# Optimization experiments

Measured on AMD Instinct MI355X. Metric: run time of the kernel, lower is better.

Reference implementation:

```python
import jax, jax.numpy as jnp
import numpy as np

# ---- static skeleton structure (SMPL 24-joint, 23-edge kinematic tree) ----
SMPL_EDGES = [[0,1],[0,2],[0,3],[1,4],[2,5],[3,6],[4,7],[5,8],[6,9],[7,10],
              [8,11],[9,12],[9,13],[9,14],[12,15],[13,16],[14,17],[16,18],
              [17,19],[18,20],[19,21],[20,22],[21,23]]
KERNEL, STRIDE, PAD, DIST = 15, 2, 7, 1

def _edge_dist(edges):
    E = len(edges)
    m = np.full((E, E), 1e6)
    np.fill_diagonal(m, 0.0)
    for i, a in enumerate(edges):
        for j, b in enumerate(edges):
            if i != j and set(a) & set(b):
                m[i, j] = 1.0
    for k in range(E):  # Floyd-Warshall on the edge adjacency graph
        m = np.minimum(m, m[:, k:k+1] + m[k:k+1, :])
    return m

def _find_neighbor(edges, d, n_global):
    m = _edge_dist(edges); E = len(edges)
    nb = [list(np.nonzero(m[i] <= d)[0]) for i in range(E)]
    gp = list(nb[0])  # edges near root edge (keeps deep-motion-editing's known quirk)
    g_ids = [E + k for k in range(n_global)]
    for i in gp:
        nb[i].extend(g_ids)
    for _ in range(n_global):
        nb.append(gp + g_ids)
    return nb

def _find_seqs(edges):
    deg = {}
    for a, b in edges:
        deg[a] = deg.get(a, 0) + 1
        deg[b] = deg.get(b, 0) + 1
    seqs = []
    def rec(j, seq):
        if deg.get(j, 0) > 2 and j != 0:
            seqs.append(seq); seq = []
        if deg.get(j, 0) == 1:
            seqs.append(seq); return
        for idx, (a, b) in enumerate(edges):
            if a == j:
                rec(b, seq + [idx])
    rec(0, [])
    return seqs

def _pooling(edges, last_pool, global_ids):
    pools, new_edges = [], []
    for seq in _find_seqs(edges):
        if last_pool:
            pools.append(seq); continue
        if len(seq) % 2 == 1:
            pools.append([seq[0]]); new_edges.append(edges[seq[0]]); seq = seq[1:]
        for i in range(0, len(seq), 2):
            pools.append([seq[i], seq[i+1]])
            new_edges.append([edges[seq[i]][0], edges[seq[i+1]][1]])
    pools.append(list(global_ids))
    return pools, new_edges

def _conv_mask(nb, in_per, out_per):
    N = len(nb)
    mask = np.zeros((N*out_per, N*in_per, 1), np.float32)
    for i, ns in enumerate(nb):
        for j in ns:
            mask[i*out_per:(i+1)*out_per, j*in_per:(j+1)*in_per, 0] = 1.0
    return mask

def _pool_matrix(pools, n_nodes, cpe):
    W = np.zeros((len(pools)*cpe, n_nodes*cpe), np.float32)
    c = np.arange(cpe)
    for i, grp in enumerate(pools):
        for j in grp:
            W[i*cpe + c, j*cpe + c] = 1.0 / len(grp)
    return W

E0 = len(SMPL_EDGES)
N0 = E0 + 2  # 23 edges + global position node + root-velocity node (the '+4' channels)
MASK0 = jnp.asarray(_conv_mask(_find_neighbor(SMPL_EDGES, DIST, 2), 4, 8))  # (200,100,1)
_pools0, EDGES1 = _pooling(SMPL_EDGES, False, [E0, E0 + 1])
P0 = jnp.asarray(_pool_matrix(_pools0, N0, 8))  # (112,200)
N1 = len(EDGES1) + 1
MASK1 = jnp.asarray(_conv_mask(_find_neighbor(EDGES1, DIST, 1), 8, 16))  # (224,112,1)
_pools1, _ = _pooling(EDGES1, True, [N1 - 1])
P1 = jnp.asarray(_pool_matrix(_pools1, N1, 16))  # (112,224)

IN0, OUT0 = 4 * N0, 8 * N0    # 100, 200
IN1, OUT1 = 8 * N1, 16 * N1   # 112, 224
B, T_IN = 64, 2047            # 2048 frames after zero-frame append


def _skel_conv(x, w, b, mask):
    # masked Conv1d (skeleton-sparse weights), stride 2, zero padding 7, k=15
    y = jax.lax.conv_general_dilated(x, w * mask, window_strides=(STRIDE,),
                                     padding=[(PAD, PAD)],
                                     dimension_numbers=('NCH', 'OIH', 'NCH'))
    return y + b[None, :, None]


def _forward(x, w0, b0, w1, b1):
    # x: (B, T, C); append one zero frame on time dim, then to (B, C, T+1)
    out = jnp.concatenate([x, jnp.zeros_like(x[:, :1, :])], axis=1)
    out = out.transpose(0, 2, 1)
    out = jax.nn.relu(jnp.einsum('pc,bct->bpt', P0, _skel_conv(out, w0, b0, MASK0)))
    out = jax.nn.relu(jnp.einsum('pc,bct->bpt', P1, _skel_conv(out, w1, b1, MASK1)))
    return out  # (B, 112, (T+1)//4)


def setup_inputs() -> dict:
    key = jax.random.key(0)
    k = jax.random.split(key, 5)
    s = 0.05
    return {
        'x':  jax.random.normal(k[0], (B, T_IN, IN0), jnp.float32),
        'w0': jax.random.normal(k[1], (OUT0, IN0, KERNEL), jnp.float32) * s,
        'b0': jax.random.normal(k[2], (OUT0,), jnp.float32) * s,
        'w1': jax.random.normal(k[3], (OUT1, IN1, KERNEL), jnp.float32) * s,
        'b1': jax.random.normal(k[4], (OUT1,), jnp.float32) * s,
    }


def reference(x, w0, b0, w1, b1):
    return _forward(x, w0, b0, w1, b1)
```

## Files before the change

kernel.cpp:

```cpp
#include <hip/hip_runtime.h>


#define OFF_A2  107520u
#define OFF_BF0 322560u
#define OFF_BF1 323008u

typedef unsigned int uint32;
typedef __attribute__((ext_vector_type(8))) short bs8;
typedef __attribute__((ext_vector_type(4))) float f32x4;
union U8 { uint4 u; bs8 s; };

__constant__ int c_pool0_len[14] = {2,2,2,2,1,2,2,1,2,2,1,2,2,2};
__constant__ int c_pool0_mem[14][2] = {{0,3},{6,9},{1,4},{7,10},{2,2},{5,8},{11,14},{12,12},
                                       {15,17},{19,21},{13,13},{16,18},{20,22},{23,24}};
__constant__ unsigned c_nbm0[25] = {
 0x180000Fu,0x1800017u,0x1800027u,0x1800049u,0x92u,0x124u,0x248u,0x490u,
 0x3920u,0x240u,0x480u,0x7900u,0xB900u,0x13900u,0x4800u,0x29000u,
 0x52000u,0xA8000u,0x150000u,0x2A0000u,0x540000u,0x280000u,0x500000u,
 0x180000Fu,0x180000Fu
};
__constant__ int c_pool1_len[7] = {2,2,2,1,3,3,1};
__constant__ int c_pool1_mem[7][3] = {{0,1,1},{2,3,3},{4,5,5},{6,6,6},{7,8,9},{10,11,12},{13,13,13}};
__constant__ unsigned c_nbm1[14] = {
 0x2017u,0x2003u,0x201Du,0xCu,0x2035u,0x4F0u,0x4E0u,0x5E0u,
 0x380u,0x300u,0xCE0u,0x1C00u,0x1800u,0x2017u
};
__constant__ int c_g1p[7][2] = {{0,13},{1,3},{2,4},{5,6},{7,10},{8,11},{9,12}};
__constant__ int c_U1[7][8] = {
 {0,1,2,3,6,23,24,25},
 {3,4,6,7,9,10,25,25},
 {0,1,2,4,5,7,23,24},
 {2,5,8,11,12,13,14,25},
 {8,11,12,13,15,16,25,25},
 {12,13,15,16,17,18,19,20},
 {17,18,19,20,21,22,25,25}};
__constant__ int c_U2[7][8] = {
 {0,1,2,4,13,14,14,14},
 {0,2,3,4,13,14,14,14},
 {0,2,4,5,6,7,10,13},
 {5,6,7,10,14,14,14,14},
 {5,6,7,8,9,10,14,14},
 {5,6,7,10,11,12,14,14},
 {0,1,2,4,13,14,14,14}};
__constant__ unsigned c_pk1a[7] = {0xC0301000u,0xC8483018u,0xB8281000u,0x70604010u,
                                   0xC8786040u,0x98887860u,0xC8A89888u};
__constant__ unsigned c_pk1b[7] = {0xC8B81808u,0xC8503820u,0xC0382008u,0xC8685828u,
                                   0xC8806858u,0xA0908068u,0xC8B0A090u};
__constant__ unsigned c_pk2[7][2] = {
 {0x40201000u,0xE0E0E0D0u},{0x40302000u,0xE0E0E0D0u},{0x50402000u,0xD0A07060u},
 {0xA0706050u,0xE0E0E0E0u},{0x80706050u,0xE0E0A090u},{0xA0706050u,0xE0E0C0B0u},
 {0x40201000u,0xE0E0E0D0u}};

__device__ __forceinline__ uint32 f2bf(float v) {
  uint32 u = __float_as_uint(v);
  return (u + 0x7fffu + ((u >> 16) & 1u)) >> 16;
}

__global__ void prep_fused_weights(const float* __restrict__ w0, const float* __restrict__ b0,
                                   const float* __restrict__ w1, const float* __restrict__ b1,
                                   char* __restrict__ wsb) {
  int t = blockIdx.x * blockDim.x + threadIdx.x;
  if (t < 6720) {
    int lane = t & 63;
    int r = t >> 6;
    int k = r % 15, g = r / 15;
    int m = lane & 15, h = lane >> 4;
    int pool = (m < 8) ? c_g1p[g][0] : c_g1p[g][1];
    int c = m & 7;
    int L = c_pool0_len[pool];
    float inv = 1.f / (float)L;
    uint32 us[8];
#pragma unroll
    for (int j = 0; j < 8; ++j) {
      int node = c_U1[g][2 * h + (j >> 2)];
      int ci = j & 3;
      float v = 0.f;
      if (node < 25) {
        for (int jj = 0; jj < L; ++jj) {
          int mem = c_pool0_mem[pool][jj];
          if ((c_nbm0[mem] >> node) & 1u)
            v += w0[(mem * 8 + c) * 1500 + (node * 4 + ci) * 15 + k];
        }
        v *= inv;
      }
      us[j] = f2bf(v);
    }
    uint4 o = make_uint4(us[0] | (us[1] << 16), us[2] | (us[3] << 16),
                         us[4] | (us[5] << 16), us[6] | (us[7] << 16));
    reinterpret_cast<uint4*>(wsb)[t] = o;
  } else if (t < 6720 + 13440) {
    int t2 = t - 6720;
    int lane = t2 & 63;
    int r = t2 >> 6;
    int k = r % 15;
    int r2 = r / 15;
    int ks = r2 & 1, p = r2 >> 1;
    int c = lane & 15, h = lane >> 4;
    int node = c_U2[p][ks * 4 + h];
    int L = c_pool1_len[p];
    float inv = 1.f / (float)L;
    uint32 us[8];
#pragma unroll
    for (int j = 0; j < 8; ++j) {
      float v = 0.f;
      if (node < 14) {
        for (int jj = 0; jj < L; ++jj) {
          int mem = c_pool1_mem[p][jj];
          if ((c_nbm1[mem] >> node) & 1u)
            v += w1[(mem * 16 + c) * 1680 + (node * 8 + j) * 15 + k];
        }
        v *= inv;
      }
      us[j] = f2bf(v);
    }
    uint4 o = make_uint4(us[0] | (us[1] << 16), us[2] | (us[3] << 16),
                         us[4] | (us[5] << 16), us[6] | (us[7] << 16));
    reinterpret_cast<uint4*>(wsb + OFF_A2)[t2] = o;
  } else if (t < 6720 + 13440 + 112) {
    int p = t - (6720 + 13440);
    int i = p >> 3, c = p & 7;
    int L = c_pool0_len[i];
    float v = 0.f;
    for (int jj = 0; jj < L; ++jj) v += b0[c_pool0_mem[i][jj] * 8 + c];
    reinterpret_cast<float*>(wsb + OFF_BF0)[p] = v / (float)L;
  } else if (t < 6720 + 13440 + 224) {
    int p = t - (6720 + 13440 + 112);
    int i = p >> 4, c = p & 15;
    int L = c_pool1_len[i];
    float v = 0.f;
    for (int jj = 0; jj < L; ++jj) v += b1[c_pool1_mem[i][jj] * 16 + c];
    reinterpret_cast<float*>(wsb + OFF_BF1)[p] = v / (float)L;
  }
}

__global__ __launch_bounds__(448, 4) void conv_fused(const float* __restrict__ x,
                                                     const char* __restrict__ wsb,
                                                     float* __restrict__ out) {
  __shared__ __align__(16) unsigned char xs[173 * 256];
  __shared__ __align__(16) unsigned char ys[80 * 256];
  const int tid = threadIdx.x;
  const int lane = tid & 63;
  const int g = tid >> 6;
  const int m16 = lane & 15, h = lane >> 4;
  const int b = blockIdx.y;
  const int t0 = blockIdx.x << 5;
  const int f0y = 2 * t0 - 7;
  const int g0x = 4 * t0 - 21;

  const float* __restrict__ xb = x + (size_t)b * (2047 * 100);
  float4 rg[10];
#pragma unroll
  for (int i = 0; i < 10; ++i) {
    rg[i] = make_float4(0.f, 0.f, 0.f, 0.f);
    int e = tid + i * 448;
    if (e < 4325) {
      int f = e / 25, q = e - f * 25;
      int gt = g0x + f;
      if ((unsigned)gt < 2047u)
        rg[i] = *reinterpret_cast<const float4*>(xb + gt * 100 + 4 * q);
    }
  }
  for (int e = tid; e < 173; e += 448)
    *reinterpret_cast<uint2*>(xs + e * 256 + (200u ^ (((e >> 1) & 15) << 3))) =
        make_uint2(0u, 0u);
#pragma unroll
  for (int i = 0; i < 10; ++i) {
    int e = tid + i * 448;
    if (e < 4325) {
      int f = e / 25, q = e - f * 25;
      uint2 w = make_uint2(f2bf(rg[i].x) | (f2bf(rg[i].y) << 16),
                           f2bf(rg[i].z) | (f2bf(rg[i].w) << 16));
      *reinterpret_cast<uint2*>(xs + f * 256 + ((q * 8) ^ (((f >> 1) & 15) << 3))) = w;
    }
  }
  const uint4* __restrict__ A1p = reinterpret_cast<const uint4*>(wsb) + g * 960 + lane;
  U8 aw[15];
#pragma unroll
  for (int k = 0; k < 15; ++k) aw[k].u = A1p[k * 64];
  const int pa = c_g1p[g][0], pb = c_g1p[g][1];
  const int chbase = (h < 2) ? (pa * 8 + 4 * h) : (pb * 8 + 4 * (h - 2));
  const float4 bv0 = *reinterpret_cast<const float4*>(wsb + OFF_BF0 + chbase * 4);
  __syncthreads();

  const uint32 offA = (c_pk1a[g] >> (8 * h)) & 255u;
  const uint32 offB = (c_pk1b[g] >> (8 * h)) & 255u;
  f32x4 acc1[5];
#pragma unroll
  for (int nt = 0; nt < 5; ++nt) acc1[nt] = (f32x4)0.f;
#pragma unroll
  for (int k = 0; k < 15; ++k) {
    const uint32 sw = (uint32)(((m16 + (k >> 1)) & 15) << 3);
    const uint32 a0 = offA ^ sw, a1o = offB ^ sw;
    const unsigned char* base = xs + (2 * m16 + k) * 256;
#pragma unroll
    for (int nt = 0; nt < 5; ++nt) {
      uint2 lo = *reinterpret_cast<const uint2*>(base + nt * 8192 + a0);
      uint2 hi = *reinterpret_cast<const uint2*>(base + nt * 8192 + a1o);
      U8 bfr; bfr.u = make_uint4(lo.x, lo.y, hi.x, hi.y);
      acc1[nt] = __builtin_amdgcn_mfma_f32_16x16x32_bf16(aw[k].s, bfr.s, acc1[nt], 0, 0, 0);
    }
  }

  const uint4* __restrict__ A2p =
      reinterpret_cast<const uint4*>(wsb + OFF_A2) + g * 1920 + lane;
#pragma unroll
  for (int k = 0; k < 15; ++k) aw[k].u = A2p[k * 64];
  const float4 bv1 = *reinterpret_cast<const float4*>(wsb + OFF_BF1 + (g * 16 + 4 * h) * 4);

#pragma unroll
  for (int nt = 0; nt < 5; ++nt) {
    int row = nt * 16 + m16;
    int fy = f0y + row;
    float o0 = fmaxf(acc1[nt][0] + bv0.x, 0.f);
    float o1 = fmaxf(acc1[nt][1] + bv0.y, 0.f);
    float o2 = fmaxf(acc1[nt][2] + bv0.z, 0.f);
    float o3 = fmaxf(acc1[nt][3] + bv0.w, 0.f);
    uint2 wpk = make_uint2(f2bf(o0) | (f2bf(o1) << 16), f2bf(o2) | (f2bf(o3) << 16));
    if ((unsigned)fy >= 1024u) wpk = make_uint2(0u, 0u);
    *reinterpret_cast<uint2*>(ys + row * 256 +
        (((uint32)(chbase * 2)) ^ (((row >> 1) & 7) << 4))) = wpk;
  }
  for (int e = tid; e < 80; e += 448)
    *reinterpret_cast<uint4*>(ys + e * 256 + (224u ^ (((e >> 1) & 7) << 4))) =
        make_uint4(0u, 0u, 0u, 0u);
  __syncthreads();

  f32x4 acc2[2];
  acc2[0] = (f32x4)0.f; acc2[1] = (f32x4)0.f;
  {
    const uint32 noff = (c_pk2[g][0] >> (8 * h)) & 255u;
#pragma unroll
    for (int k = 0; k < 15; ++k) {
      const uint32 sw = (uint32)(((m16 + (k >> 1)) & 7) << 4);
      const unsigned char* base = ys + 2 * m16 * 256 + (noff ^ sw);
      U8 b0f, b1f;
      b0f.u = *reinterpret_cast<const uint4*>(base + k * 256);
      b1f.u = *reinterpret_cast<const uint4*>(base + (k + 32) * 256);
      acc2[0] = __builtin_amdgcn_mfma_f32_16x16x32_bf16(aw[k].s, b0f.s, acc2[0], 0, 0, 0);
      acc2[1] = __builtin_amdgcn_mfma_f32_16x16x32_bf16(aw[k].s, b1f.s, acc2[1], 0, 0, 0);
    }
  }
#pragma unroll
  for (int k = 0; k < 15; ++k) aw[k].u = A2p[(15 + k) * 64];
  {
    const uint32 noff = (c_pk2[g][1] >> (8 * h)) & 255u;
#pragma unroll
    for (int k = 0; k < 15; ++k) {
      const uint32 sw = (uint32)(((m16 + (k >> 1)) & 7) << 4);
      const unsigned char* base = ys + 2 * m16 * 256 + (noff ^ sw);
      U8 b0f, b1f;
      b0f.u = *reinterpret_cast<const uint4*>(base + k * 256);
      b1f.u = *reinterpret_cast<const uint4*>(base + (k + 32) * 256);
      acc2[0] = __builtin_amdgcn_mfma_f32_16x16x32_bf16(aw[k].s, b0f.s, acc2[0], 0, 0, 0);
      acc2[1] = __builtin_amdgcn_mfma_f32_16x16x32_bf16(aw[k].s, b1f.s, acc2[1], 0, 0, 0);
    }
  }

#pragma unroll
  for (int nt = 0; nt < 2; ++nt) {
    size_t obase = ((size_t)b * 112 + g * 16 + 4 * h) * 512 + t0 + nt * 16 + m16;
    out[obase]        = fmaxf(acc2[nt][0] + bv1.x, 0.f);
    out[obase + 512]  = fmaxf(acc2[nt][1] + bv1.y, 0.f);
    out[obase + 1024] = fmaxf(acc2[nt][2] + bv1.z, 0.f);
    out[obase + 1536] = fmaxf(acc2[nt][3] + bv1.w, 0.f);
  }
}

extern "C" void kernel_launch(void* const* d_in, const int* in_sizes, int n_in,
                              void* d_out, int out_size, void* d_ws, size_t ws_size,
                              hipStream_t stream) {
  const float* x  = (const float*)d_in[0];
  const float* w0 = (const float*)d_in[1];
  const float* b0 = (const float*)d_in[2];
  const float* w1 = (const float*)d_in[3];
  const float* b1 = (const float*)d_in[4];
  char* wsb = (char*)d_ws;
  float* out = (float*)d_out;

  prep_fused_weights<<<80, 256, 0, stream>>>(w0, b0, w1, b1, wsb);
  conv_fused<<<dim3(16, 64), 448, 0, stream>>>(x, wsb, out);
}
```

Measured before the change: 53.72 us.

## Process two time tiles per block with prefetched input and staged coalesced stores

```diff
diff --git a/kernel.cpp b/kernel.cpp
--- a/kernel.cpp
+++ b/kernel.cpp
@@ -133,136 +133,158 @@
   }
 }
 
+#define GATHER(T0VAL)                                                          \
+  do {                                                                         \
+    const int gg = 4 * (T0VAL) - 21;                                           \
+    _Pragma("unroll")                                                          \
+    for (int i = 0; i < 10; ++i) {                                             \
+      rg[i] = make_float4(0.f, 0.f, 0.f, 0.f);                                 \
+      int e = tid + i * 448;                                                   \
+      if (e < 4325) {                                                          \
+        int f = e / 25, q = e - f * 25;                                        \
+        int gt = gg + f;                                                       \
+        if ((unsigned)gt < 2047u)                                              \
+          rg[i] = *reinterpret_cast<const float4*>(xb + gt * 100 + 4 * q);     \
+      }                                                                        \
+    }                                                                          \
+  } while (0)
+
 __global__ __launch_bounds__(448, 4) void conv_fused(const float* __restrict__ x,
                                                      const char* __restrict__ wsb,
                                                      float* __restrict__ out) {
   __shared__ __align__(16) unsigned char xs[173 * 256];
   __shared__ __align__(16) unsigned char ys[80 * 256];
+  float* const ysf = reinterpret_cast<float*>(ys);
   const int tid = threadIdx.x;
   const int lane = tid & 63;
   const int g = tid >> 6;
   const int m16 = lane & 15, h = lane >> 4;
   const int b = blockIdx.y;
-  const int t0 = blockIdx.x << 5;
-  const int f0y = 2 * t0 - 7;
-  const int g0x = 4 * t0 - 21;
-
   const float* __restrict__ xb = x + (size_t)b * (2047 * 100);
-  float4 rg[10];
-#pragma unroll
-  for (int i = 0; i < 10; ++i) {
-    rg[i] = make_float4(0.f, 0.f, 0.f, 0.f);
-    int e = tid + i * 448;
-    if (e < 4325) {
-      int f = e / 25, q = e - f * 25;
-      int gt = g0x + f;
-      if ((unsigned)gt < 2047u)
-        rg[i] = *reinterpret_cast<const float4*>(xb + gt * 100 + 4 * q);
-    }
-  }
-  for (int e = tid; e < 173; e += 448)
-    *reinterpret_cast<uint2*>(xs + e * 256 + (200u ^ (((e >> 1) & 15) << 3))) =
-        make_uint2(0u, 0u);
-#pragma unroll
-  for (int i = 0; i < 10; ++i) {
-    int e = tid + i * 448;
-    if (e < 4325) {
-      int f = e / 25, q = e - f * 25;
-      uint2 w = make_uint2(f2bf(rg[i].x) | (f2bf(rg[i].y) << 16),
-                           f2bf(rg[i].z) | (f2bf(rg[i].w) << 16));
-      *reinterpret_cast<uint2*>(xs + f * 256 + ((q * 8) ^ (((f >> 1) & 15) << 3))) = w;
-    }
-  }
+
   const uint4* __restrict__ A1p = reinterpret_cast<const uint4*>(wsb) + g * 960 + lane;
-  U8 aw[15];
-#pragma unroll
-  for (int k = 0; k < 15; ++k) aw[k].u = A1p[k * 64];
+  const uint4* __restrict__ A2p =
+      reinterpret_cast<const uint4*>(wsb + OFF_A2) + g * 1920 + lane;
   const int pa = c_g1p[g][0], pb = c_g1p[g][1];
   const int chbase = (h < 2) ? (pa * 8 + 4 * h) : (pb * 8 + 4 * (h - 2));
   const float4 bv0 = *reinterpret_cast<const float4*>(wsb + OFF_BF0 + chbase * 4);
-  __syncthreads();
-
+  const float4 bv1 = *reinterpret_cast<const float4*>(wsb + OFF_BF1 + (g * 16 + 4 * h) * 4);
   const uint32 offA = (c_pk1a[g] >> (8 * h)) & 255u;
   const uint32 offB = (c_pk1b[g] >> (8 * h)) & 255u;
-  f32x4 acc1[5];
-#pragma unroll
-  for (int nt = 0; nt < 5; ++nt) acc1[nt] = (f32x4)0.f;
-#pragma unroll
-  for (int k = 0; k < 15; ++k) {
-    const uint32 sw = (uint32)(((m16 + (k >> 1)) & 15) << 3);
-    const uint32 a0 = offA ^ sw, a1o = offB ^ sw;
-    const unsigned char* base = xs + (2 * m16 + k) * 256;
+
+  float4 rg[10];
+  GATHER(blockIdx.x * 64);
+
+  for (int it = 0; it < 2; ++it) {
+    const int t0 = blockIdx.x * 64 + it * 32;
+    const int f0y = 2 * t0 - 7;
+
+    for (int e = tid; e < 173; e += 448)
+      *reinterpret_cast<uint2*>(xs + e * 256 + (200u ^ (((e >> 1) & 15) << 3))) =
+          make_uint2(0u, 0u);
+#pragma unroll
+    for (int i = 0; i < 10; ++i) {
+      int e = tid + i * 448;
+      if (e < 4325) {
+        int f = e / 25, q = e - f * 25;
+        uint2 w = make_uint2(f2bf(rg[i].x) | (f2bf(rg[i].y) << 16),
+                             f2bf(rg[i].z) | (f2bf(rg[i].w) << 16));
+        *reinterpret_cast<uint2*>(xs + f * 256 + ((q * 8) ^ (((f >> 1) & 15) << 3))) = w;
+      }
+    }
+    U8 aw[15];
+#pragma unroll
+    for (int k = 0; k < 15; ++k) aw[k].u = A1p[k * 64];
+    __syncthreads();
+
+    f32x4 acc1[5];
+#pragma unroll
+    for (int nt = 0; nt < 5; ++nt) acc1[nt] = (f32x4)0.f;
+#pragma unroll
+    for (int k = 0; k < 15; ++k) {
+      const uint32 sw = (uint32)(((m16 + (k >> 1)) & 15) << 3);
+      const uint32 a0 = offA ^ sw, a1o = offB ^ sw;
+      const unsigned char* base = xs + (2 * m16 + k) * 256;
+#pragma unroll
+      for (int nt = 0; nt < 5; ++nt) {
+        uint2 lo = *reinterpret_cast<const uint2*>(base + nt * 8192 + a0);
+        uint2 hi = *reinterpret_cast<const uint2*>(base + nt * 8192 + a1o);
+        U8 bfr; bfr.u = make_uint4(lo.x, lo.y, hi.x, hi.y);
+        acc1[nt] = __builtin_amdgcn_mfma_f32_16x16x32_bf16(aw[k].s, bfr.s, acc1[nt], 0, 0, 0);
+      }
+    }
+
+#pragma unroll
+    for (int k = 0; k < 15; ++k) aw[k].u = A2p[k * 64];
+
 #pragma unroll
     for (int nt = 0; nt < 5; ++nt) {
-      uint2 lo = *reinterpret_cast<const uint2*>(base + nt * 8192 + a0);
-      uint2 hi = *reinterpret_cast<const uint2*>(base + nt * 8192 + a1o);
-      U8 bfr; bfr.u = make_uint4(lo.x, lo.y, hi.x, hi.y);
-      acc1[nt] = __builtin_amdgcn_mfma_f32_16x16x32_bf16(aw[k].s, bfr.s, acc1[nt], 0, 0, 0);
-    }
-  }
-
-  const uint4* __restrict__ A2p =
-      reinterpret_cast<const uint4*>(wsb + OFF_A2) + g * 1920 + lane;
-#pragma unroll
-  for (int k = 0; k < 15; ++k) aw[k].u = A2p[k * 64];
-  const float4 bv1 = *reinterpret_cast<const float4*>(wsb + OFF_BF1 + (g * 16 + 4 * h) * 4);
-
-#pragma unroll
-  for (int nt = 0; nt < 5; ++nt) {
-    int row = nt * 16 + m16;
-    int fy = f0y + row;
-    float o0 = fmaxf(acc1[nt][0] + bv0.x, 0.f);
-    float o1 = fmaxf(acc1[nt][1] + bv0.y, 0.f);
-    float o2 = fmaxf(acc1[nt][2] + bv0.z, 0.f);
-    float o3 = fmaxf(acc1[nt][3] + bv0.w, 0.f);
-    uint2 wpk = make_uint2(f2bf(o0) | (f2bf(o1) << 16), f2bf(o2) | (f2bf(o3) << 16));
-    if ((unsigned)fy >= 1024u) wpk = make_uint2(0u, 0u);
-    *reinterpret_cast<uint2*>(ys + row * 256 +
-        (((uint32)(chbase * 2)) ^ (((row >> 1) & 7) << 4))) = wpk;
-  }
-  for (int e = tid; e < 80; e += 448)
-    *reinterpret_cast<uint4*>(ys + e * 256 + (224u ^ (((e >> 1) & 7) << 4))) =
-        make_uint4(0u, 0u, 0u, 0u);
-  __syncthreads();
-
-  f32x4 acc2[2];
-  acc2[0] = (f32x4)0.f; acc2[1] = (f32x4)0.f;
-  {
-    const uint32 noff = (c_pk2[g][0] >> (8 * h)) & 255u;
-#pragma unroll
-    for (int k = 0; k < 15; ++k) {
-      const uint32 sw = (uint32)(((m16 + (k >> 1)) & 7) << 4);
-      const unsigned char* base = ys + 2 * m16 * 256 + (noff ^ sw);
-      U8 b0f, b1f;
-      b0f.u = *reinterpret_cast<const uint4*>(base + k * 256);
-      b1f.u = *reinterpret_cast<const uint4*>(base + (k + 32) * 256);
-      acc2[0] = __builtin_amdgcn_mfma_f32_16x16x32_bf16(aw[k].s, b0f.s, acc2[0], 0, 0, 0);
-      acc2[1] = __builtin_amdgcn_mfma_f32_16x16x32_bf16(aw[k].s, b1f.s, acc2[1], 0, 0, 0);
-    }
-  }
-#pragma unroll
-  for (int k = 0; k < 15; ++k) aw[k].u = A2p[(15 + k) * 64];
-  {
-    const uint32 noff = (c_pk2[g][1] >> (8 * h)) & 255u;
-#pragma unroll
-    for (int k = 0; k < 15; ++k) {
-      const uint32 sw = (uint32)(((m16 + (k >> 1)) & 7) << 4);
-      const unsigned char* base = ys + 2 * m16 * 256 + (noff ^ sw);
-      U8 b0f, b1f;
-      b0f.u = *reinterpret_cast<const uint4*>(base + k * 256);
-      b1f.u = *reinterpret_cast<const uint4*>(base + (k + 32) * 256);
-      acc2[0] = __builtin_amdgcn_mfma_f32_16x16x32_bf16(aw[k].s, b0f.s, acc2[0], 0, 0, 0);
-      acc2[1] = __builtin_amdgcn_mfma_f32_16x16x32_bf16(aw[k].s, b1f.s, acc2[1], 0, 0, 0);
-    }
-  }
-
-#pragma unroll
-  for (int nt = 0; nt < 2; ++nt) {
-    size_t obase = ((size_t)b * 112 + g * 16 + 4 * h) * 512 + t0 + nt * 16 + m16;
-    out[obase]        = fmaxf(acc2[nt][0] + bv1.x, 0.f);
-    out[obase + 512]  = fmaxf(acc2[nt][1] + bv1.y, 0.f);
-    out[obase + 1024] = fmaxf(acc2[nt][2] + bv1.z, 0.f);
-    out[obase + 1536] = fmaxf(acc2[nt][3] + bv1.w, 0.f);
+      int row = nt * 16 + m16;
+      int fy = f0y + row;
+      float o0 = fmaxf(acc1[nt][0] + bv0.x, 0.f);
+      float o1 = fmaxf(acc1[nt][1] + bv0.y, 0.f);
+      float o2 = fmaxf(acc1[nt][2] + bv0.z, 0.f);
+      float o3 = fmaxf(acc1[nt][3] + bv0.w, 0.f);
+      uint2 wpk = make_uint2(f2bf(o0) | (f2bf(o1) << 16), f2bf(o2) | (f2bf(o3) << 16));
+      if ((unsigned)fy >= 1024u) wpk = make_uint2(0u, 0u);
+      *reinterpret_cast<uint2*>(ys + row * 256 +
+          (((uint32)(chbase * 2)) ^ (((row >> 1) & 7) << 4))) = wpk;
+    }
+    for (int e = tid; e < 80; e += 448)
+      *reinterpret_cast<uint4*>(ys + e * 256 + (224u ^ (((e >> 1) & 7) << 4))) =
+          make_uint4(0u, 0u, 0u, 0u);
+    __syncthreads();
+
+    if (it == 0) GATHER(blockIdx.x * 64 + 32);
+
+    f32x4 acc2[2];
+    acc2[0] = (f32x4)0.f; acc2[1] = (f32x4)0.f;
+    {
+      const uint32 noff = (c_pk2[g][0] >> (8 * h)) & 255u;
+#pragma unroll
+      for (int k = 0; k < 15; ++k) {
+        const uint32 sw = (uint32)(((m16 + (k >> 1)) & 7) << 4);
+        const unsigned char* base = ys + 2 * m16 * 256 + (noff ^ sw);
+        U8 b0f, b1f;
+        b0f.u = *reinterpret_cast<const uint4*>(base + k * 256);
+        b1f.u = *reinterpret_cast<const uint4*>(base + (k + 32) * 256);
+        acc2[0] = __builtin_amdgcn_mfma_f32_16x16x32_bf16(aw[k].s, b0f.s, acc2[0], 0, 0, 0);
+        acc2[1] = __builtin_amdgcn_mfma_f32_16x16x32_bf16(aw[k].s, b1f.s, acc2[1], 0, 0, 0);
+      }
+    }
+#pragma unroll
+    for (int k = 0; k < 15; ++k) aw[k].u = A2p[(15 + k) * 64];
+    {
+      const uint32 noff = (c_pk2[g][1] >> (8 * h)) & 255u;
+#pragma unroll
+      for (int k = 0; k < 15; ++k) {
+        const uint32 sw = (uint32)(((m16 + (k >> 1)) & 7) << 4);
+        const unsigned char* base = ys + 2 * m16 * 256 + (noff ^ sw);
+        U8 b0f, b1f;
+        b0f.u = *reinterpret_cast<const uint4*>(base + k * 256);
+        b1f.u = *reinterpret_cast<const uint4*>(base + (k + 32) * 256);
+        acc2[0] = __builtin_amdgcn_mfma_f32_16x16x32_bf16(aw[k].s, b0f.s, acc2[0], 0, 0, 0);
+        acc2[1] = __builtin_amdgcn_mfma_f32_16x16x32_bf16(aw[k].s, b1f.s, acc2[1], 0, 0, 0);
+      }
+    }
+    __syncthreads();
+
+#pragma unroll
+    for (int nt = 0; nt < 2; ++nt) {
+      int t = nt * 16 + m16;
+      ysf[(g * 16 + 4 * h + 0) * 36 + t] = fmaxf(acc2[nt][0] + bv1.x, 0.f);
+      ysf[(g * 16 + 4 * h + 1) * 36 + t] = fmaxf(acc2[nt][1] + bv1.y, 0.f);
+      ysf[(g * 16 + 4 * h + 2) * 36 + t] = fmaxf(acc2[nt][2] + bv1.z, 0.f);
+      ysf[(g * 16 + 4 * h + 3) * 36 + t] = fmaxf(acc2[nt][3] + bv1.w, 0.f);
+    }
+    __syncthreads();
+#pragma unroll
+    for (int r = 0; r < 2; ++r) {
+      int e = tid + r * 448;
+      int ch = e >> 3, jj = e & 7;
+      float4 v = *reinterpret_cast<const float4*>(ysf + ch * 36 + jj * 4);
+      *reinterpret_cast<float4*>(out + ((size_t)b * 112 + ch) * 512 + t0 + jj * 4) = v;
+    }
   }
 }
 
@@ -278,5 +300,5 @@
   float* out = (float*)d_out;
 
   prep_fused_weights<<<80, 256, 0, stream>>>(w0, b0, w1, b1, wsb);
-  conv_fused<<<dim3(16, 64), 448, 0, stream>>>(x, wsb, out);
+  conv_fused<<<dim3(8, 64), 448, 0, stream>>>(x, wsb, out);
 }
```

After: 183.9 us. +242.3%, slower.

## Halve time tile per block and stage output through LDS for vector stores

Applied to the files above, without the earlier changes.

```diff
diff --git a/kernel.cpp b/kernel.cpp
--- a/kernel.cpp
+++ b/kernel.cpp
@@ -136,37 +136,38 @@
 __global__ __launch_bounds__(448, 4) void conv_fused(const float* __restrict__ x,
                                                      const char* __restrict__ wsb,
                                                      float* __restrict__ out) {
-  __shared__ __align__(16) unsigned char xs[173 * 256];
-  __shared__ __align__(16) unsigned char ys[80 * 256];
+  __shared__ __align__(16) unsigned char xs[109 * 256];
+  __shared__ __align__(16) unsigned char ys[48 * 256];
+  float* const ysf = reinterpret_cast<float*>(ys);
   const int tid = threadIdx.x;
   const int lane = tid & 63;
   const int g = tid >> 6;
   const int m16 = lane & 15, h = lane >> 4;
   const int b = blockIdx.y;
-  const int t0 = blockIdx.x << 5;
+  const int t0 = blockIdx.x << 4;
   const int f0y = 2 * t0 - 7;
   const int g0x = 4 * t0 - 21;
-
   const float* __restrict__ xb = x + (size_t)b * (2047 * 100);
-  float4 rg[10];
-#pragma unroll
-  for (int i = 0; i < 10; ++i) {
+
+  float4 rg[7];
+#pragma unroll
+  for (int i = 0; i < 7; ++i) {
     rg[i] = make_float4(0.f, 0.f, 0.f, 0.f);
     int e = tid + i * 448;
-    if (e < 4325) {
+    if (e < 2725) {
       int f = e / 25, q = e - f * 25;
       int gt = g0x + f;
       if ((unsigned)gt < 2047u)
         rg[i] = *reinterpret_cast<const float4*>(xb + gt * 100 + 4 * q);
     }
   }
-  for (int e = tid; e < 173; e += 448)
+  for (int e = tid; e < 109; e += 448)
     *reinterpret_cast<uint2*>(xs + e * 256 + (200u ^ (((e >> 1) & 15) << 3))) =
         make_uint2(0u, 0u);
 #pragma unroll
-  for (int i = 0; i < 10; ++i) {
+  for (int i = 0; i < 7; ++i) {
     int e = tid + i * 448;
-    if (e < 4325) {
+    if (e < 2725) {
       int f = e / 25, q = e - f * 25;
       uint2 w = make_uint2(f2bf(rg[i].x) | (f2bf(rg[i].y) << 16),
                            f2bf(rg[i].z) | (f2bf(rg[i].w) << 16));
@@ -184,16 +185,16 @@
 
   const uint32 offA = (c_pk1a[g] >> (8 * h)) & 255u;
   const uint32 offB = (c_pk1b[g] >> (8 * h)) & 255u;
-  f32x4 acc1[5];
-#pragma unroll
-  for (int nt = 0; nt < 5; ++nt) acc1[nt] = (f32x4)0.f;
+  f32x4 acc1[3];
+#pragma unroll
+  for (int nt = 0; nt < 3; ++nt) acc1[nt] = (f32x4)0.f;
 #pragma unroll
   for (int k = 0; k < 15; ++k) {
     const uint32 sw = (uint32)(((m16 + (k >> 1)) & 15) << 3);
     const uint32 a0 = offA ^ sw, a1o = offB ^ sw;
     const unsigned char* base = xs + (2 * m16 + k) * 256;
 #pragma unroll
-    for (int nt = 0; nt < 5; ++nt) {
+    for (int nt = 0; nt < 3; ++nt) {
       uint2 lo = *reinterpret_cast<const uint2*>(base + nt * 8192 + a0);
       uint2 hi = *reinterpret_cast<const uint2*>(base + nt * 8192 + a1o);
       U8 bfr; bfr.u = make_uint4(lo.x, lo.y, hi.x, hi.y);
@@ -208,7 +209,7 @@
   const float4 bv1 = *reinterpret_cast<const float4*>(wsb + OFF_BF1 + (g * 16 + 4 * h) * 4);
 
 #pragma unroll
-  for (int nt = 0; nt < 5; ++nt) {
+  for (int nt = 0; nt < 3; ++nt) {
     int row = nt * 16 + m16;
     int fy = f0y + row;
     float o0 = fmaxf(acc1[nt][0] + bv0.x, 0.f);
@@ -220,24 +221,20 @@
     *reinterpret_cast<uint2*>(ys + row * 256 +
         (((uint32)(chbase * 2)) ^ (((row >> 1) & 7) << 4))) = wpk;
   }
-  for (int e = tid; e < 80; e += 448)
+  for (int e = tid; e < 48; e += 448)
     *reinterpret_cast<uint4*>(ys + e * 256 + (224u ^ (((e >> 1) & 7) << 4))) =
         make_uint4(0u, 0u, 0u, 0u);
   __syncthreads();
 
-  f32x4 acc2[2];
-  acc2[0] = (f32x4)0.f; acc2[1] = (f32x4)0.f;
+  f32x4 acc2 = (f32x4)0.f;
   {
     const uint32 noff = (c_pk2[g][0] >> (8 * h)) & 255u;
 #pragma unroll
     for (int k = 0; k < 15; ++k) {
       const uint32 sw = (uint32)(((m16 + (k >> 1)) & 7) << 4);
-      const unsigned char* base = ys + 2 * m16 * 256 + (noff ^ sw);
-      U8 b0f, b1f;
-      b0f.u = *reinterpret_cast<const uint4*>(base + k * 256);
-      b1f.u = *reinterpret_cast<const uint4*>(base + (k + 32) * 256);
-      acc2[0] = __builtin_amdgcn_mfma_f32_16x16x32_bf16(aw[k].s, b0f.s, acc2[0], 0, 0, 0);
-      acc2[1] = __builtin_amdgcn_mfma_f32_16x16x32_bf16(aw[k].s, b1f.s, acc2[1], 0, 0, 0);
+      U8 bf;
+      bf.u = *reinterpret_cast<const uint4*>(ys + (2 * m16 + k) * 256 + (noff ^ sw));
+      acc2 = __builtin_amdgcn_mfma_f32_16x16x32_bf16(aw[k].s, bf.s, acc2, 0, 0, 0);
     }
   }
 #pragma unroll
@@ -247,22 +244,25 @@
 #pragma unroll
     for (int k = 0; k < 15; ++k) {
       const uint32 sw = (uint32)(((m16 + (k >> 1)) & 7) << 4);
-      const unsigned char* base = ys + 2 * m16 * 256 + (noff ^ sw);
-      U8 b0f, b1f;
-      b0f.u = *reinterpret_cast<const uint4*>(base + k * 256);
-      b1f.u = *reinterpret_cast<const uint4*>(base + (k + 32) * 256);
-      acc2[0] = __builtin_amdgcn_mfma_f32_16x16x32_bf16(aw[k].s, b0f.s, acc2[0], 0, 0, 0);
-      acc2[1] = __builtin_amdgcn_mfma_f32_16x16x32_bf16(aw[k].s, b1f.s, acc2[1], 0, 0, 0);
-    }
-  }
-
-#pragma unroll
-  for (int nt = 0; nt < 2; ++nt) {
-    size_t obase = ((size_t)b * 112 + g * 16 + 4 * h) * 512 + t0 + nt * 16 + m16;
-    out[obase]        = fmaxf(acc2[nt][0] + bv1.x, 0.f);
-    out[obase + 512]  = fmaxf(acc2[nt][1] + bv1.y, 0.f);
-    out[obase + 1024] = fmaxf(acc2[nt][2] + bv1.z, 0.f);
-    out[obase + 1536] = fmaxf(acc2[nt][3] + bv1.w, 0.f);
+      U8 bf;
+      bf.u = *reinterpret_cast<const uint4*>(ys + (2 * m16 + k) * 256 + (noff ^ sw));
+      acc2 = __builtin_amdgcn_mfma_f32_16x16x32_bf16(aw[k].s, bf.s, acc2, 0, 0, 0);
+    }
+  }
+  __syncthreads();
+
+  {
+    int t = m16;
+    ysf[(g * 16 + 4 * h + 0) * 20 + t] = fmaxf(acc2[0] + bv1.x, 0.f);
+    ysf[(g * 16 + 4 * h + 1) * 20 + t] = fmaxf(acc2[1] + bv1.y, 0.f);
+    ysf[(g * 16 + 4 * h + 2) * 20 + t] = fmaxf(acc2[2] + bv1.z, 0.f);
+    ysf[(g * 16 + 4 * h + 3) * 20 + t] = fmaxf(acc2[3] + bv1.w, 0.f);
+  }
+  __syncthreads();
+  {
+    int ch = tid >> 2, jj = tid & 3;
+    float4 v = *reinterpret_cast<const float4*>(ysf + ch * 20 + jj * 4);
+    *reinterpret_cast<float4*>(out + ((size_t)b * 112 + ch) * 512 + t0 + jj * 4) = v;
   }
 }
 
@@ -278,5 +278,5 @@
   float* out = (float*)d_out;
 
   prep_fused_weights<<<80, 256, 0, stream>>>(w0, b0, w1, b1, wsb);
-  conv_fused<<<dim3(16, 64), 448, 0, stream>>>(x, wsb, out);
-}
+  conv_fused<<<dim3(32, 64), 448, 0, stream>>>(x, wsb, out);
+}
```

Result: slower. 61.97 us (+15.3%).
